# Performance work log

Measured on AMD Instinct MI355X. Metric: run time of the kernel, lower is better.

The kernel has to match this reference:

```python
import jax, jax.numpy as jnp
import numpy as np

N = 50000      # nodes
E = 600000     # edges
F_IN = 128     # input features
H = 128        # hidden
C = 40         # classes


def _glorot(key, shape):
    lim = float(np.sqrt(6.0 / (shape[0] + shape[1])))
    return jax.random.uniform(key, shape, jnp.float32, -lim, lim)


def setup_inputs() -> dict:
    key = jax.random.key(0)
    ks = jax.random.split(key, 16)
    inp = {
        "x": jax.random.normal(ks[0], (N, F_IN), jnp.float32),
        "edge_index": jax.random.randint(ks[1], (2, E), 0, N, jnp.int64),
    }
    # SAGEConv params: Wl (neighbor branch, with bias), Wr (root branch), stored [in, out]
    dims = [(F_IN, H), (H, H), (H, H)]
    for i, (din, dout) in enumerate(dims, start=1):
        inp[f"Wl{i}"] = _glorot(ks[2 * i], (din, dout))
        inp[f"bl{i}"] = jnp.zeros((dout,), jnp.float32)
        inp[f"Wr{i}"] = _glorot(ks[2 * i + 1], (din, dout))
    inp["W_lin1"] = _glorot(ks[10], (H, H))
    inp["b_lin1"] = jnp.zeros((H,), jnp.float32)
    inp["W_lin2"] = _glorot(ks[11], (H, C))
    inp["b_lin2"] = jnp.zeros((C,), jnp.float32)
    return inp


def _sage_conv(x, src, dst, Wl, bl, Wr):
    # mean-aggregate neighbor features at destination nodes
    msgs = x[src]  # [E, d] gather
    agg = jax.ops.segment_sum(msgs, dst, num_segments=N)
    deg = jax.ops.segment_sum(jnp.ones((E,), x.dtype), dst, num_segments=N)
    agg = agg / jnp.clip(deg, 1.0)[:, None]
    return agg @ Wl + bl + x @ Wr


def reference(x, edge_index, Wl1, bl1, Wr1, Wl2, bl2, Wr2, Wl3, bl3, Wr3,
              W_lin1, b_lin1, W_lin2, b_lin2):
    src, dst = edge_index[0], edge_index[1]
    h = jax.nn.relu(_sage_conv(x, src, dst, Wl1, bl1, Wr1))
    h = jax.nn.relu(_sage_conv(h, src, dst, Wl2, bl2, Wr2))
    h = jax.nn.relu(_sage_conv(h, src, dst, Wl3, bl3, Wr3))
    h = jax.nn.relu(h @ W_lin1 + b_lin1)
    # dropout: inference mode (training=False) -> identity
    logits = h @ W_lin2 + b_lin2
    return jax.nn.log_softmax(logits, axis=-1)
```

## Files before the change

kernel.cpp:

```cpp
#include <hip/hip_runtime.h>
#include <hip/hip_bf16.h>
#include <math.h>

#define NNODES 50000
#define NEDGES 600000
#define FDIM   128
#define NCLS   40
#define SLOTS  64
#define FILL_BLOCKS 2344
#define CVT_BLOCKS 6251
#define S1_TOTAL (FILL_BLOCKS + CVT_BLOCKS + 62)
#define NT16 (NNODES / 16)

typedef __hip_bfloat16 bf16;
typedef short bf16x8 __attribute__((ext_vector_type(8)));
typedef short bf16x4 __attribute__((ext_vector_type(4)));
typedef float f32x4  __attribute__((ext_vector_type(4)));

__device__ __forceinline__ float b2f(short u) {
    union { unsigned int i; float f; } cv;
    cv.i = ((unsigned int)(unsigned short)u) << 16;
    return cv.f;
}
__device__ __forceinline__ short f2b(float f) {
    bf16 h = __float2bfloat16(f);
    return *(const short*)&h;
}
__device__ __forceinline__ int edge_val(const int* e32, const long long* e64,
                                        int is64, int idx) {
    return is64 ? (int)e64[idx] : e32[idx];
}
__device__ __forceinline__ float ldf(const void* p, int fp32, int idx) {
    return fp32 ? ((const float*)p)[idx]
                : __bfloat162float(((const bf16*)p)[idx]);
}
__device__ __forceinline__ int lidx(int row, int col) {
    return row * 128 + ((((col >> 3) ^ (row & 15)) << 3) | (col & 7));
}

struct MP {
    const int* e32; const long long* e64;
    const void* xin;
    const void *Wl1, *Wr1, *Wl2, *Wr2, *Wl3, *Wr3, *Wlin1, *Wlin2;
    const void *b1, *b2, *b3, *b4, *b5;
    int *cursor, *flags, *edge_src;
    bf16x8* packed; float* biasf;
    bf16 *xb, *bufA;
    float* out;
};

__device__ __forceinline__ void detect_body(int b, int tid, const unsigned int* ei,
        const unsigned int* xp, const unsigned int* wp, int* flags, int* cnt) {
    if (tid == 0) *cnt = 0;
    __syncthreads();
    if (b == 0) {
        int nz = 0;
        for (int i = tid; i < 2048; i += 256) if (ei[2 * i + 1] != 0u) nz++;
        atomicAdd(cnt, nz);
        __syncthreads();
        if (tid == 0) flags[1] = (*cnt == 0) ? 1 : 0;
    } else {
        const unsigned int* pp = (b == 1) ? xp : wp;
        int inr = 0;
        for (int i = tid; i < 2048; i += 256) {
            unsigned int e = (pp[i] >> 7) & 0xFFu;
            if (e >= 100u && e <= 140u) inr++;
        }
        atomicAdd(cnt, inr);
        __syncthreads();
        if (tid == 0) flags[b + 1] = (*cnt < 1024) ? 1 : 0;
    }
}

__global__ void k_init_f(const unsigned int* ei, const unsigned int* xp,
                         const unsigned int* wp, int* flags, int* cursor,
                         int* edge_src, bf16* bufA) {
    __shared__ int cnt;
    int b = blockIdx.x, tid = threadIdx.x, B = gridDim.x;
    if (b < 3) detect_body(b, tid, ei, xp, wp, flags, &cnt);
    if (b == 3 && tid < 32)
        ((uint2*)(bufA + (size_t)NNODES * FDIM))[tid] = (uint2){0u, 0u};
    for (int i = b * 256 + tid; i < NNODES; i += B * 256) cursor[i] = 0;
    int4 sent = (int4){NNODES, NNODES, NNODES, NNODES};
    for (int i = b * 256 + tid; i < NNODES * (SLOTS / 4); i += B * 256)
        ((int4*)edge_src)[i] = sent;
}

__device__ __forceinline__ void stage1_body(int vb, int tid, const MP& p,
                                            int is64, int xf, int wf) {
    if (vb < FILL_BLOCKS) {
        int i = vb * 256 + tid;
        if (i < NEDGES) {
            int srcn = edge_val(p.e32, p.e64, is64, i);
            int dstn = edge_val(p.e32, p.e64, is64, NEDGES + i);
            int pos = atomicAdd(&p.cursor[dstn], 1);
            if (pos < SLOTS) p.edge_src[dstn * SLOTS + pos] = srcn;
        }
        return;
    }
    if (vb < FILL_BLOCKS + CVT_BLOCKS) {
        int i = (vb - FILL_BLOCKS) * 256 + tid;
        if (i >= (NNODES + 1) * FDIM / 4) return;
        if (i >= NNODES * FDIM / 4) {
            bf16x4 z = (bf16x4){0, 0, 0, 0};
            ((bf16x4*)p.xb)[i] = z;
        } else if (xf) {
            float4 v = ((const float4*)p.xin)[i];
            bf16x4 o;
            o[0] = f2b(v.x); o[1] = f2b(v.y); o[2] = f2b(v.z); o[3] = f2b(v.w);
            ((bf16x4*)p.xb)[i] = o;
        } else {
            ((uint2*)p.xb)[i] = ((const uint2*)p.xin)[i];
        }
        return;
    }
    int lb = vb - FILL_BLOCKS - CVT_BLOCKS;
    if (lb >= 59) {
        int t = (lb - 59) * 256 + tid;
        if (t >= 5 * 128) return;
        int which = t >> 7, idx = t & 127;
        const void* srcs[5] = {p.b1, p.b2, p.b3, p.b4, p.b5};
        int n = (which == 4) ? NCLS : 128;
        float v = 0.f;
        if (idx < n) v = ldf(srcs[which], wf, idx);
        p.biasf[t] = v;
        return;
    }
    int t2 = lb * 256 + tid;
    int frag = t2 >> 6, lane = t2 & 63;
    if (frag >= 236) return;
    int q = lane >> 4, l16 = lane & 15;
    const void* W;
    int kbase, n, ldw = 128, nvalid = 128;
    if (frag < 192) {
        int g = frag >> 6, local = frag & 63;
        int kt = local >> 3, nt = local & 7;
        const void* Wl = (g == 0) ? p.Wl1 : (g == 1) ? p.Wl2 : p.Wl3;
        const void* Wr = (g == 0) ? p.Wr1 : (g == 1) ? p.Wr2 : p.Wr3;
        W = (kt < 4) ? Wl : Wr;
        kbase = (kt & 3) * 32;
        n = nt * 16 + l16;
    } else if (frag < 224) {
        int local = frag - 192;
        int kt = local >> 3, nt = local & 7;
        W = p.Wlin1; kbase = kt * 32; n = nt * 16 + l16;
    } else {
        int local = frag - 224;
        int kt = local / 3, nt = local % 3;
        W = p.Wlin2; kbase = kt * 32; n = nt * 16 + l16;
        ldw = NCLS; nvalid = NCLS;
    }
    bf16x8 v;
#pragma unroll
    for (int j = 0; j < 8; j++) {
        float e = 0.f;
        if (n < nvalid) e = ldf(W, wf, (kbase + q * 8 + j) * ldw + n);
        v[j] = f2b(e);
    }
    p.packed[frag * 64 + lane] = v;
}
__global__ void k_stage1_f(MP p) {
    stage1_body(blockIdx.x, threadIdx.x, p, p.flags[1], p.flags[2], p.flags[3]);
}

__device__ __forceinline__ void agg_wave(const bf16* __restrict__ x,
        const int* __restrict__ deg, const int* __restrict__ edge_src,
        short* __restrict__ lds, int rowbase, int wave, int lane) {
    const int g = lane >> 4, c = lane & 15;
    const int base = rowbase + wave * 8;
    int dgv = deg[base];
    int eidx = edge_src[base * SLOTS + lane];
#pragma unroll
    for (int t = 0; t < 8; t++) {
        int dgn = 0;
        bool haveN = (t < 7);
        if (haveN) dgn = deg[base + t + 1];
        int dcap = dgv < SLOTS ? ((dgv + 15) & ~15) : SLOTS;
        float acc[8];
#pragma unroll
        for (int e = 0; e < 8; e++) acc[e] = 0.f;
        for (int i = 0; i < dcap; i += 16) {
            unsigned o0 = (unsigned)(__shfl(eidx, i + g)      * FDIM + c * 8);
            unsigned o1 = (unsigned)(__shfl(eidx, i + 4 + g)  * FDIM + c * 8);
            unsigned o2 = (unsigned)(__shfl(eidx, i + 8 + g)  * FDIM + c * 8);
            unsigned o3 = (unsigned)(__shfl(eidx, i + 12 + g) * FDIM + c * 8);
            bf16x8 v0 = *(const bf16x8*)(x + o0);
            bf16x8 v1 = *(const bf16x8*)(x + o1);
            bf16x8 v2 = *(const bf16x8*)(x + o2);
            bf16x8 v3 = *(const bf16x8*)(x + o3);
#pragma unroll
            for (int e = 0; e < 8; e++)
                acc[e] += (b2f(v0[e]) + b2f(v1[e])) + (b2f(v2[e]) + b2f(v3[e]));
        }
        int en = 0;
        if (haveN) en = edge_src[(base + t + 1) * SLOTS + lane];
#pragma unroll
        for (int e = 0; e < 8; e++) {
            float a = acc[e];
            a += __shfl_xor(a, 16);
            a += __shfl_xor(a, 32);
            acc[e] = a;
        }
        if (g == 0) {
            float inv = (dgv > 0) ? 1.f / (float)dgv : 0.f;
            bf16x8 o;
#pragma unroll
            for (int e = 0; e < 8; e++) o[e] = f2b(acc[e] * inv);
            *(bf16x8*)(lds + lidx(wave * 8 + t, c * 8)) = o;
        }
        dgv = dgn; eidx = en;
    }
}

template <bool TO_LDS>
__device__ __forceinline__ void gemm_phase(int rowbase, int lane, int wave,
        short* __restrict__ aggL, const bf16* __restrict__ xroot,
        const bf16x8* __restrict__ packed, const float* __restrict__ bias,
        bf16* __restrict__ out) {
    const int q = lane >> 4, l16 = lane & 15;
    const unsigned rowA = (unsigned)(rowbase + l16);
    f32x4 acc[4];
#pragma unroll
    for (int n = 0; n < 4; n++) acc[n] = (f32x4){0.f, 0.f, 0.f, 0.f};
#pragma unroll 2
    for (int kt = 0; kt < 8; kt++) {
        bf16x8 a;
        if (kt < 4)
            a = *(const bf16x8*)(aggL + lidx(l16, kt * 32 + q * 8));
        else
            a = *(const bf16x8*)(xroot + rowA * FDIM + (kt - 4) * 32 + q * 8);
        bf16x8 b[4];
#pragma unroll
        for (int n = 0; n < 4; n++)
            b[n] = packed[(kt * 8 + wave * 4 + n) * 64 + lane];
#pragma unroll
        for (int n = 0; n < 4; n++)
            acc[n] = __builtin_amdgcn_mfma_f32_16x16x32_bf16(a, b[n], acc[n], 0, 0, 0);
    }
    if (TO_LDS) __syncthreads();
#pragma unroll
    for (int n = 0; n < 4; n++) {
        int col = (wave * 4 + n) * 16 + l16;
        float bv = bias[col];
#pragma unroll
        for (int r = 0; r < 4; r++) {
            float v = fmaxf(acc[n][r] + bv, 0.f);
            if (TO_LDS)
                aggL[lidx(q * 4 + r, col)] = f2b(v);
            else
                out[(unsigned)(rowbase + q * 4 + r) * FDIM + col] = __float2bfloat16(v);
        }
    }
}

__device__ __forceinline__ void head_phase(int rowbase, int lane, int wave,
        const short* __restrict__ h3, short* __restrict__ h1,
        const bf16x8* __restrict__ packed, const float* __restrict__ bias1,
        const float* __restrict__ bias2, float* __restrict__ out) {
    const int q = lane >> 4, l16 = lane & 15;
    f32x4 acc[4];
#pragma unroll
    for (int n = 0; n < 4; n++) acc[n] = (f32x4){0.f, 0.f, 0.f, 0.f};
#pragma unroll 2
    for (int kt = 0; kt < 4; kt++) {
        bf16x8 a = *(const bf16x8*)(h3 + lidx(l16, kt * 32 + q * 8));
        bf16x8 b[4];
#pragma unroll
        for (int n = 0; n < 4; n++)
            b[n] = packed[(192 + kt * 8 + wave * 4 + n) * 64 + lane];
#pragma unroll
        for (int n = 0; n < 4; n++)
            acc[n] = __builtin_amdgcn_mfma_f32_16x16x32_bf16(a, b[n], acc[n], 0, 0, 0);
    }
#pragma unroll
    for (int n = 0; n < 4; n++) {
        int col = (wave * 4 + n) * 16 + l16;
        float bv = bias1[col];
#pragma unroll
        for (int r = 0; r < 4; r++)
            h1[lidx(q * 4 + r, col)] = f2b(fmaxf(acc[n][r] + bv, 0.f));
    }
    __syncthreads();
    if (wave >= 1) return;
    f32x4 acc2[3];
#pragma unroll
    for (int n = 0; n < 3; n++) acc2[n] = (f32x4){0.f, 0.f, 0.f, 0.f};
#pragma unroll
    for (int kt = 0; kt < 4; kt++) {
        bf16x8 a = *(const bf16x8*)(h1 + lidx(l16, kt * 32 + q * 8));
        bf16x8 b[3];
#pragma unroll
        for (int n = 0; n < 3; n++) b[n] = packed[(224 + kt * 3 + n) * 64 + lane];
#pragma unroll
        for (int n = 0; n < 3; n++)
            acc2[n] = __builtin_amdgcn_mfma_f32_16x16x32_bf16(a, b[n], acc2[n], 0, 0, 0);
    }
    const float NEG = -1e30f;
    bool v2ok = (l16 < 8);
#pragma unroll
    for (int r = 0; r < 4; r++) {
        unsigned row = (unsigned)(rowbase + q * 4 + r);
        float v0 = acc2[0][r] + bias2[l16];
        float v1 = acc2[1][r] + bias2[16 + l16];
        float v2 = v2ok ? (acc2[2][r] + bias2[32 + l16]) : NEG;
        float m = fmaxf(fmaxf(v0, v1), v2);
#pragma unroll
        for (int mk = 1; mk < 16; mk <<= 1) m = fmaxf(m, __shfl_xor(m, mk));
        float sden = expf(v0 - m) + expf(v1 - m) + (v2ok ? expf(v2 - m) : 0.f);
#pragma unroll
        for (int mk = 1; mk < 16; mk <<= 1) sden += __shfl_xor(sden, mk);
        float l = m + logf(sden);
        out[row * NCLS + l16] = v0 - l;
        out[row * NCLS + 16 + l16] = v1 - l;
        if (v2ok) out[row * NCLS + 32 + l16] = v2 - l;
    }
}

__global__ void __launch_bounds__(128)
k_layer(const bf16* __restrict__ src, const int* __restrict__ deg,
        const int* __restrict__ edge_src, const bf16x8* __restrict__ packed,
        const float* __restrict__ bias, bf16* __restrict__ out) {
    __shared__ __align__(16) short aggL[16 * 128];
    const int lane = threadIdx.x & 63, wave = threadIdx.x >> 6;
    const int rowbase = blockIdx.x * 16;
    agg_wave(src, deg, edge_src, aggL, rowbase, wave, lane);
    __syncthreads();
    gemm_phase<false>(rowbase, lane, wave, aggL, src, packed, bias, out);
}

__global__ void __launch_bounds__(128)
k_layer3head(const bf16* __restrict__ src, const int* __restrict__ deg,
             const int* __restrict__ edge_src, const bf16x8* __restrict__ packed,
             const float* __restrict__ biasf, float* __restrict__ out) {
    __shared__ __align__(16) short aggL[16 * 128];
    __shared__ __align__(16) short h1[16 * 128];
    const int lane = threadIdx.x & 63, wave = threadIdx.x >> 6;
    const int rowbase = blockIdx.x * 16;
    agg_wave(src, deg, edge_src, aggL, rowbase, wave, lane);
    __syncthreads();
    gemm_phase<true>(rowbase, lane, wave, aggL, src, packed + 128 * 64,
                     biasf + 256, nullptr);
    __syncthreads();
    head_phase(rowbase, lane, wave, aggL, h1, packed, biasf + 384, biasf + 512, out);
}

extern "C" void kernel_launch(void* const* d_in, const int* in_sizes, int n_in,
                              void* d_out, int out_size, void* d_ws, size_t ws_size,
                              hipStream_t stream) {
    char* ws = (char*)d_ws;
    size_t off = 0;
    auto take = [&](size_t bytes) {
        void* pp = ws + off;
        off = (off + bytes + 255) & ~(size_t)255;
        return pp;
    };
    MP p;
    p.e32 = (const int*)d_in[1];
    p.e64 = (const long long*)d_in[1];
    p.xin = d_in[0];
    p.Wl1 = d_in[2];  p.Wr1 = d_in[4];
    p.Wl2 = d_in[5];  p.Wr2 = d_in[7];
    p.Wl3 = d_in[8];  p.Wr3 = d_in[10];
    p.Wlin1 = d_in[11]; p.Wlin2 = d_in[13];
    p.b1 = d_in[3]; p.b2 = d_in[6]; p.b3 = d_in[9]; p.b4 = d_in[12]; p.b5 = d_in[14];
    p.cursor   = (int*)take(NNODES * 4);
    p.flags    = (int*)take(256);
    p.edge_src = (int*)take((size_t)NNODES * SLOTS * 4);
    p.packed   = (bf16x8*)take(236 * 64 * 16);
    p.biasf    = (float*)take(5 * 128 * 4);
    p.xb       = (bf16*)take((size_t)(NNODES + 1) * FDIM * 2);
    p.bufA     = (bf16*)take((size_t)(NNODES + 1) * FDIM * 2);
    p.out      = (float*)d_out;
    bf16* bufB = p.xb;

    k_init_f<<<512, 256, 0, stream>>>((const unsigned int*)d_in[1],
                                      (const unsigned int*)d_in[0],
                                      (const unsigned int*)d_in[2],
                                      p.flags, p.cursor, p.edge_src, p.bufA);
    k_stage1_f<<<S1_TOTAL, 256, 0, stream>>>(p);

    k_layer<<<NT16, 128, 0, stream>>>(p.xb, p.cursor, p.edge_src,
                                      p.packed, p.biasf, p.bufA);
    k_layer<<<NT16, 128, 0, stream>>>(p.bufA, p.cursor, p.edge_src,
                                      p.packed + 64 * 64, p.biasf + 128, bufB);
    k_layer3head<<<NT16, 128, 0, stream>>>(bufB, p.cursor, p.edge_src,
                                           p.packed, p.biasf, p.out);
}
```

Measured before the change: 257.0 us.

## Drop sentinel fill of edge slots; mask padded neighbors and detect dtypes per wave

Removes the init kernel that wrote sentinel values into the whole 50000x64 edge-slot table and zeroed a padding row. Instead, the aggregation clamps unwritten slot indices to node 0 and multiplies their contribution by a zero mask. Dtype detection now uses wave ballots inside each kernel, so the flags buffer and its dependency are gone. The cursor zeroing moves into the prep kernel, ahead of a separate fill kernel. This saves a large memset-like pass in exchange for extra mask FMAs in the gather loop and reads of uninitialized slot memory.

```diff
diff --git a/kernel.cpp b/kernel.cpp
--- a/kernel.cpp
+++ b/kernel.cpp
@@ -7,9 +7,10 @@
 #define FDIM   128
 #define NCLS   40
 #define SLOTS  64
-#define FILL_BLOCKS 2344
-#define CVT_BLOCKS 6251
-#define S1_TOTAL (FILL_BLOCKS + CVT_BLOCKS + 62)
+#define CVT_BLOCKS 6250
+#define PACK_BLOCKS 62
+#define CZ_BLOCKS 196
+#define PREP_TOTAL (CVT_BLOCKS + PACK_BLOCKS + CZ_BLOCKS)
 #define NT16 (NNODES / 16)
 
 typedef __hip_bfloat16 bf16;
@@ -26,108 +27,62 @@
     bf16 h = __float2bfloat16(f);
     return *(const short*)&h;
 }
-__device__ __forceinline__ int edge_val(const int* e32, const long long* e64,
-                                        int is64, int idx) {
-    return is64 ? (int)e64[idx] : e32[idx];
-}
 __device__ __forceinline__ float ldf(const void* p, int fp32, int idx) {
     return fp32 ? ((const float*)p)[idx]
                 : __bfloat162float(((const bf16*)p)[idx]);
 }
+__device__ __forceinline__ int wave_is_fp32(const unsigned* p, int lane) {
+    unsigned w = p[lane];
+    unsigned e = (w >> 7) & 0xFFu;
+    int inr = (e >= 100u && e <= 140u) ? 1 : 0;
+    return (int)__popcll(__ballot(inr)) < 32;
+}
 __device__ __forceinline__ int lidx(int row, int col) {
     return row * 128 + ((((col >> 3) ^ (row & 15)) << 3) | (col & 7));
 }
 
-struct MP {
-    const int* e32; const long long* e64;
-    const void* xin;
-    const void *Wl1, *Wr1, *Wl2, *Wr2, *Wl3, *Wr3, *Wlin1, *Wlin2;
-    const void *b1, *b2, *b3, *b4, *b5;
-    int *cursor, *flags, *edge_src;
-    bf16x8* packed; float* biasf;
-    bf16 *xb, *bufA;
-    float* out;
-};
-
-__device__ __forceinline__ void detect_body(int b, int tid, const unsigned int* ei,
-        const unsigned int* xp, const unsigned int* wp, int* flags, int* cnt) {
-    if (tid == 0) *cnt = 0;
-    __syncthreads();
-    if (b == 0) {
-        int nz = 0;
-        for (int i = tid; i < 2048; i += 256) if (ei[2 * i + 1] != 0u) nz++;
-        atomicAdd(cnt, nz);
-        __syncthreads();
-        if (tid == 0) flags[1] = (*cnt == 0) ? 1 : 0;
-    } else {
-        const unsigned int* pp = (b == 1) ? xp : wp;
-        int inr = 0;
-        for (int i = tid; i < 2048; i += 256) {
-            unsigned int e = (pp[i] >> 7) & 0xFFu;
-            if (e >= 100u && e <= 140u) inr++;
-        }
-        atomicAdd(cnt, inr);
-        __syncthreads();
-        if (tid == 0) flags[b + 1] = (*cnt < 1024) ? 1 : 0;
-    }
-}
-
-__global__ void k_init_f(const unsigned int* ei, const unsigned int* xp,
-                         const unsigned int* wp, int* flags, int* cursor,
-                         int* edge_src, bf16* bufA) {
-    __shared__ int cnt;
-    int b = blockIdx.x, tid = threadIdx.x, B = gridDim.x;
-    if (b < 3) detect_body(b, tid, ei, xp, wp, flags, &cnt);
-    if (b == 3 && tid < 32)
-        ((uint2*)(bufA + (size_t)NNODES * FDIM))[tid] = (uint2){0u, 0u};
-    for (int i = b * 256 + tid; i < NNODES; i += B * 256) cursor[i] = 0;
-    int4 sent = (int4){NNODES, NNODES, NNODES, NNODES};
-    for (int i = b * 256 + tid; i < NNODES * (SLOTS / 4); i += B * 256)
-        ((int4*)edge_src)[i] = sent;
-}
-
-__device__ __forceinline__ void stage1_body(int vb, int tid, const MP& p,
-                                            int is64, int xf, int wf) {
-    if (vb < FILL_BLOCKS) {
-        int i = vb * 256 + tid;
-        if (i < NEDGES) {
-            int srcn = edge_val(p.e32, p.e64, is64, i);
-            int dstn = edge_val(p.e32, p.e64, is64, NEDGES + i);
-            int pos = atomicAdd(&p.cursor[dstn], 1);
-            if (pos < SLOTS) p.edge_src[dstn * SLOTS + pos] = srcn;
-        }
-        return;
-    }
-    if (vb < FILL_BLOCKS + CVT_BLOCKS) {
-        int i = (vb - FILL_BLOCKS) * 256 + tid;
-        if (i >= (NNODES + 1) * FDIM / 4) return;
-        if (i >= NNODES * FDIM / 4) {
-            bf16x4 z = (bf16x4){0, 0, 0, 0};
-            ((bf16x4*)p.xb)[i] = z;
-        } else if (xf) {
-            float4 v = ((const float4*)p.xin)[i];
+__global__ void k_prep(const void* __restrict__ xin,
+                       const void* Wl1, const void* Wr1, const void* Wl2,
+                       const void* Wr2, const void* Wl3, const void* Wr3,
+                       const void* Wlin1, const void* Wlin2,
+                       const void* b1, const void* b2, const void* b3,
+                       const void* b4, const void* b5,
+                       int* __restrict__ cursor, bf16* __restrict__ xb,
+                       bf16x8* __restrict__ packed, float* __restrict__ biasf) {
+    int b = blockIdx.x, tid = threadIdx.x, lane = tid & 63;
+    if (b < CVT_BLOCKS) {
+        int xf = wave_is_fp32((const unsigned*)xin, lane);
+        int i = b * 256 + tid;
+        if (xf) {
+            float4 v = ((const float4*)xin)[i];
             bf16x4 o;
             o[0] = f2b(v.x); o[1] = f2b(v.y); o[2] = f2b(v.z); o[3] = f2b(v.w);
-            ((bf16x4*)p.xb)[i] = o;
+            ((bf16x4*)xb)[i] = o;
         } else {
-            ((uint2*)p.xb)[i] = ((const uint2*)p.xin)[i];
+            ((uint2*)xb)[i] = ((const uint2*)xin)[i];
         }
         return;
     }
-    int lb = vb - FILL_BLOCKS - CVT_BLOCKS;
+    if (b >= CVT_BLOCKS + PACK_BLOCKS) {
+        int i = (b - CVT_BLOCKS - PACK_BLOCKS) * 256 + tid;
+        if (i < NNODES) cursor[i] = 0;
+        return;
+    }
+    int wf = wave_is_fp32((const unsigned*)Wl1, lane);
+    int lb = b - CVT_BLOCKS;
     if (lb >= 59) {
         int t = (lb - 59) * 256 + tid;
         if (t >= 5 * 128) return;
         int which = t >> 7, idx = t & 127;
-        const void* srcs[5] = {p.b1, p.b2, p.b3, p.b4, p.b5};
+        const void* srcs[5] = {b1, b2, b3, b4, b5};
         int n = (which == 4) ? NCLS : 128;
         float v = 0.f;
         if (idx < n) v = ldf(srcs[which], wf, idx);
-        p.biasf[t] = v;
+        biasf[t] = v;
         return;
     }
     int t2 = lb * 256 + tid;
-    int frag = t2 >> 6, lane = t2 & 63;
+    int frag = t2 >> 6;
     if (frag >= 236) return;
     int q = lane >> 4, l16 = lane & 15;
     const void* W;
@@ -135,19 +90,19 @@
     if (frag < 192) {
         int g = frag >> 6, local = frag & 63;
         int kt = local >> 3, nt = local & 7;
-        const void* Wl = (g == 0) ? p.Wl1 : (g == 1) ? p.Wl2 : p.Wl3;
-        const void* Wr = (g == 0) ? p.Wr1 : (g == 1) ? p.Wr2 : p.Wr3;
+        const void* Wl = (g == 0) ? Wl1 : (g == 1) ? Wl2 : Wl3;
+        const void* Wr = (g == 0) ? Wr1 : (g == 1) ? Wr2 : Wr3;
         W = (kt < 4) ? Wl : Wr;
         kbase = (kt & 3) * 32;
         n = nt * 16 + l16;
     } else if (frag < 224) {
         int local = frag - 192;
         int kt = local >> 3, nt = local & 7;
-        W = p.Wlin1; kbase = kt * 32; n = nt * 16 + l16;
+        W = Wlin1; kbase = kt * 32; n = nt * 16 + l16;
     } else {
         int local = frag - 224;
         int kt = local / 3, nt = local % 3;
-        W = p.Wlin2; kbase = kt * 32; n = nt * 16 + l16;
+        W = Wlin2; kbase = kt * 32; n = nt * 16 + l16;
         ldw = NCLS; nvalid = NCLS;
     }
     bf16x8 v;
@@ -157,10 +112,20 @@
         if (n < nvalid) e = ldf(W, wf, (kbase + q * 8 + j) * ldw + n);
         v[j] = f2b(e);
     }
-    p.packed[frag * 64 + lane] = v;
-}
-__global__ void k_stage1_f(MP p) {
-    stage1_body(blockIdx.x, threadIdx.x, p, p.flags[1], p.flags[2], p.flags[3]);
+    packed[frag * 64 + lane] = v;
+}
+
+__global__ void k_fill(const int* __restrict__ e32, const long long* __restrict__ e64,
+                       int* __restrict__ cursor, int* __restrict__ edge_src) {
+    int lane = threadIdx.x & 63;
+    unsigned hw = ((const unsigned*)e32)[2 * lane + 1];
+    int is64 = (__ballot(hw != 0u) == 0ull) ? 1 : 0;
+    int i = blockIdx.x * 256 + threadIdx.x;
+    if (i >= NEDGES) return;
+    int srcn = is64 ? (int)e64[i] : e32[i];
+    int dstn = is64 ? (int)e64[NEDGES + i] : e32[NEDGES + i];
+    int pos = atomicAdd(&cursor[dstn], 1);
+    if (pos < SLOTS) edge_src[dstn * SLOTS + pos] = srcn;
 }
 
 __device__ __forceinline__ void agg_wave(const bf16* __restrict__ x,
@@ -170,16 +135,20 @@
     const int base = rowbase + wave * 8;
     int dgv = deg[base];
     int eidx = edge_src[base * SLOTS + lane];
+    if ((unsigned)eidx >= NNODES) eidx = 0;
 #pragma unroll
     for (int t = 0; t < 8; t++) {
         int dgn = 0;
-        bool haveN = (t < 7);
-        if (haveN) dgn = deg[base + t + 1];
+        if (t < 7) dgn = deg[base + t + 1];
         int dcap = dgv < SLOTS ? ((dgv + 15) & ~15) : SLOTS;
         float acc[8];
 #pragma unroll
         for (int e = 0; e < 8; e++) acc[e] = 0.f;
         for (int i = 0; i < dcap; i += 16) {
+            float m0 = (i + g < dgv) ? 1.f : 0.f;
+            float m1 = (i + 4 + g < dgv) ? 1.f : 0.f;
+            float m2 = (i + 8 + g < dgv) ? 1.f : 0.f;
+            float m3 = (i + 12 + g < dgv) ? 1.f : 0.f;
             unsigned o0 = (unsigned)(__shfl(eidx, i + g)      * FDIM + c * 8);
             unsigned o1 = (unsigned)(__shfl(eidx, i + 4 + g)  * FDIM + c * 8);
             unsigned o2 = (unsigned)(__shfl(eidx, i + 8 + g)  * FDIM + c * 8);
@@ -189,11 +158,18 @@
             bf16x8 v2 = *(const bf16x8*)(x + o2);
             bf16x8 v3 = *(const bf16x8*)(x + o3);
 #pragma unroll
-            for (int e = 0; e < 8; e++)
-                acc[e] += (b2f(v0[e]) + b2f(v1[e])) + (b2f(v2[e]) + b2f(v3[e]));
+            for (int e = 0; e < 8; e++) {
+                acc[e] = fmaf(b2f(v0[e]), m0, acc[e]);
+                acc[e] = fmaf(b2f(v1[e]), m1, acc[e]);
+                acc[e] = fmaf(b2f(v2[e]), m2, acc[e]);
+                acc[e] = fmaf(b2f(v3[e]), m3, acc[e]);
+            }
         }
         int en = 0;
-        if (haveN) en = edge_src[(base + t + 1) * SLOTS + lane];
+        if (t < 7) {
+            en = edge_src[(base + t + 1) * SLOTS + lane];
+            if ((unsigned)en >= NNODES) en = 0;
+        }
 #pragma unroll
         for (int e = 0; e < 8; e++) {
             float a = acc[e];
@@ -354,35 +330,26 @@
         off = (off + bytes + 255) & ~(size_t)255;
         return pp;
     };
-    MP p;
-    p.e32 = (const int*)d_in[1];
-    p.e64 = (const long long*)d_in[1];
-    p.xin = d_in[0];
-    p.Wl1 = d_in[2];  p.Wr1 = d_in[4];
-    p.Wl2 = d_in[5];  p.Wr2 = d_in[7];
-    p.Wl3 = d_in[8];  p.Wr3 = d_in[10];
-    p.Wlin1 = d_in[11]; p.Wlin2 = d_in[13];
-    p.b1 = d_in[3]; p.b2 = d_in[6]; p.b3 = d_in[9]; p.b4 = d_in[12]; p.b5 = d_in[14];
-    p.cursor   = (int*)take(NNODES * 4);
-    p.flags    = (int*)take(256);
-    p.edge_src = (int*)take((size_t)NNODES * SLOTS * 4);
-    p.packed   = (bf16x8*)take(236 * 64 * 16);
-    p.biasf    = (float*)take(5 * 128 * 4);
-    p.xb       = (bf16*)take((size_t)(NNODES + 1) * FDIM * 2);
-    p.bufA     = (bf16*)take((size_t)(NNODES + 1) * FDIM * 2);
-    p.out      = (float*)d_out;
-    bf16* bufB = p.xb;
-
-    k_init_f<<<512, 256, 0, stream>>>((const unsigned int*)d_in[1],
-                                      (const unsigned int*)d_in[0],
-                                      (const unsigned int*)d_in[2],
-                                      p.flags, p.cursor, p.edge_src, p.bufA);
-    k_stage1_f<<<S1_TOTAL, 256, 0, stream>>>(p);
-
-    k_layer<<<NT16, 128, 0, stream>>>(p.xb, p.cursor, p.edge_src,
-                                      p.packed, p.biasf, p.bufA);
-    k_layer<<<NT16, 128, 0, stream>>>(p.bufA, p.cursor, p.edge_src,
-                                      p.packed + 64 * 64, p.biasf + 128, bufB);
-    k_layer3head<<<NT16, 128, 0, stream>>>(bufB, p.cursor, p.edge_src,
-                                           p.packed, p.biasf, p.out);
-}
+    const int* e32 = (const int*)d_in[1];
+    const long long* e64 = (const long long*)d_in[1];
+    int* cursor    = (int*)take(NNODES * 4);
+    int* edge_src  = (int*)take((size_t)NNODES * SLOTS * 4);
+    bf16x8* packed = (bf16x8*)take(236 * 64 * 16);
+    float* biasf   = (float*)take(5 * 128 * 4);
+    bf16* xb       = (bf16*)take((size_t)NNODES * FDIM * 2);
+    bf16* bufA     = (bf16*)take((size_t)NNODES * FDIM * 2);
+    float* outp    = (float*)d_out;
+    bf16* bufB     = xb;
+
+    k_prep<<<PREP_TOTAL, 256, 0, stream>>>(
+        d_in[0], d_in[2], d_in[4], d_in[5], d_in[7], d_in[8], d_in[10],
+        d_in[11], d_in[13], d_in[3], d_in[6], d_in[9], d_in[12], d_in[14],
+        cursor, xb, packed, biasf);
+    k_fill<<<(NEDGES + 255) / 256, 256, 0, stream>>>(e32, e64, cursor, edge_src);
+
+    k_layer<<<NT16, 128, 0, stream>>>(xb, cursor, edge_src, packed, biasf, bufA);
+    k_layer<<<NT16, 128, 0, stream>>>(bufA, cursor, edge_src,
+                                      packed + 64 * 64, biasf + 128, bufB);
+    k_layer3head<<<NT16, 128, 0, stream>>>(bufB, cursor, edge_src,
+                                           packed, biasf, outp);
+}
```

New measurement: 248.2 us. 3.4% less time.
